# Optimization experiments

Measured on AMD Instinct MI355X. Metric: run time of the kernel, lower is better.

Reference implementation:

```python
import jax, jax.numpy as jnp
import numpy as np

VOCAB, EMBED_DIM, ENCODE_DIM = 50000, 128, 128
B, N = 512, 500            # trees per batch, nodes per tree
MAX_DEPTH = 40             # static bound on tree depth (uniform-attachment trees stay far below)


def setup_inputs() -> dict:
    rng = np.random.default_rng(0)
    T = B * N
    tokens = rng.integers(0, VOCAB, size=T).astype(np.int64)
    # random recursive trees: node i attaches to a uniformly random earlier node
    u = rng.random((B, N))
    pl = np.floor(u * np.arange(N)).astype(np.int64)  # local parent; node 0 is root
    depth = np.zeros((B, N), dtype=np.int64)
    rows = np.arange(B)
    for i in range(1, N):
        depth[:, i] = depth[rows, pl[:, i]] + 1
    assert depth.max() < MAX_DEPTH
    parent = pl + (np.arange(B)[:, None] * N)
    parent[:, 0] = T  # roots scatter into a dummy row
    node2batch = np.repeat(np.arange(B), N).astype(np.int64)

    key = jax.random.key(0)
    k1, k2, k3 = jax.random.split(key, 3)
    emb = jax.random.normal(k1, (VOCAB, EMBED_DIM), jnp.float32) * 0.02
    Wc = jax.random.normal(k2, (EMBED_DIM, ENCODE_DIM), jnp.float32) * 0.05
    bc = jax.random.normal(k3, (ENCODE_DIM,), jnp.float32) * 0.01
    return {
        "tokens": jnp.asarray(tokens),
        "parent": jnp.asarray(parent.reshape(-1)),
        "depth": jnp.asarray(depth.reshape(-1)),
        "node2batch": jnp.asarray(node2batch),
        "emb": emb, "Wc": Wc, "bc": bc, "bs": B,
    }


def reference(tokens, parent, depth, node2batch, emb, Wc, bc, bs):
    T = tokens.shape[0]
    # per-node W_c(embedding(token))  [T, D]
    x = emb[tokens] @ Wc + bc
    # bottom-up subtree sums: v(n) = sum_{m in subtree(n)} x[m]
    v = jnp.concatenate([x, jnp.zeros((1, x.shape[1]), x.dtype)], axis=0)  # +1 dummy row
    for d in range(MAX_DEPTH, 0, -1):
        contrib = jnp.where((depth == d)[:, None], v[:T], jnp.zeros((), x.dtype))
        v = v.at[parent].add(contrib)  # depth-d nodes push into depth d-1 parents
    node_vals = v[:T]
    # per-tree elementwise max over node values (node_list max-pool)
    out = jax.ops.segment_max(node_vals, node2batch, num_segments=bs)
    # rows absent from a node_list entry are zero, so the pool includes 0
    return jnp.maximum(out, jnp.zeros((), out.dtype))
```

## Files before the change

### kernel.cpp

```cpp
#include <hip/hip_runtime.h>
#include <hip/hip_bf16.h>

#define B_BATCH 512
#define NPB     500
#define DIM     128
#define VOCAB   50000
#define MAXD    40
#define NPREP   512
#define NGEMM   ((VOCAB + 63) / 64)

typedef short bf16x8 __attribute__((ext_vector_type(8)));
typedef float f32x4  __attribute__((ext_vector_type(4)));

__device__ __forceinline__ unsigned short f2bf(float x) {
    unsigned u = __float_as_uint(x);
    return (unsigned short)((u + 0x7fffu + ((u >> 16) & 1u)) >> 16);
}

__global__ __launch_bounds__(256, 3) void prep_gemm(const int* __restrict__ tokens,
                                                    const int* __restrict__ parent,
                                                    const int* __restrict__ depth,
                                                    const float* __restrict__ emb,
                                                    const float* __restrict__ Wc,
                                                    const float* __restrict__ bc,
                                                    int* __restrict__ tokD,
                                                    unsigned short* __restrict__ endD,
                                                    float* __restrict__ E) {
    __shared__ __align__(16) char smem[50176];
    const int tid = threadIdx.x;

    if (blockIdx.x >= NPREP) {
        unsigned short* sA = (unsigned short*)smem;
        unsigned short* sB = (unsigned short*)(smem + 17408);
        const int rowBase = (blockIdx.x - NPREP) * 64;

        for (int i = tid; i < DIM * DIM; i += 256) {
            int k = i >> 7, n = i & 127;
            int kc = k >> 5, q = (k >> 3) & 3, jj = k & 7;
            int nt = n >> 4, ln = q * 16 + (n & 15);
            sB[((kc * 8 + nt) * 64 + ln) * 8 + jj] = f2bf(Wc[i]);
        }
        for (int i = tid; i < 64 * 32; i += 256) {
            int r = i >> 5, k4 = (i & 31) * 4;
            float4 v = make_float4(0.f, 0.f, 0.f, 0.f);
            if (rowBase + r < VOCAB)
                v = *(const float4*)&emb[(long long)(rowBase + r) * DIM + k4];
            unsigned long long pk =  (unsigned long long)f2bf(v.x)
                                  | ((unsigned long long)f2bf(v.y) << 16)
                                  | ((unsigned long long)f2bf(v.z) << 32)
                                  | ((unsigned long long)f2bf(v.w) << 48);
            *(unsigned long long*)&sA[r * 136 + k4] = pk;
        }
        __syncthreads();

        const int lane = tid & 63, w = tid >> 6;
        const int q = lane >> 4, mc = lane & 15;

        f32x4 acc[8];
        #pragma unroll
        for (int nt = 0; nt < 8; ++nt) acc[nt] = (f32x4){0.f, 0.f, 0.f, 0.f};

        #pragma unroll
        for (int kc = 0; kc < 4; ++kc) {
            bf16x8 a = *(const bf16x8*)&sA[(w * 16 + mc) * 136 + kc * 32 + q * 8];
            #pragma unroll
            for (int nt = 0; nt < 8; ++nt) {
                bf16x8 bf = *(const bf16x8*)&sB[((kc * 8 + nt) * 64 + lane) * 8];
                acc[nt] = __builtin_amdgcn_mfma_f32_16x16x32_bf16(a, bf, acc[nt], 0, 0, 0);
            }
        }

        #pragma unroll
        for (int nt = 0; nt < 8; ++nt) {
            float bcv = bc[nt * 16 + mc];
            #pragma unroll
            for (int r = 0; r < 4; ++r) {
                int grow = rowBase + w * 16 + q * 4 + r;
                if (grow < VOCAB)
                    E[(long long)grow * DIM + nt * 16 + mc] = acc[nt][r] + bcv;
            }
        }
        return;
    }

    int*            sizeL  = (int*)smem;
    int*            pack   = (int*)(smem + 2000);
    int*            tokL   = (int*)(smem + 4000);
    int*            tmpTok = (int*)(smem + 6000);
    int*            hist   = (int*)(smem + 8000);
    int*            off    = (int*)(smem + 8164);
    int*            cur    = (int*)(smem + 8328);
    int*            sdmax  = (int*)(smem + 8492);
    unsigned short* parL   = (unsigned short*)(smem + 8496);
    unsigned short* depL   = (unsigned short*)(smem + 9496);
    unsigned short* sibp   = (unsigned short*)(smem + 10496);
    unsigned short* tinL   = (unsigned short*)(smem + 11496);
    unsigned short* bucket = (unsigned short*)(smem + 12496);
    unsigned short* tmpEnd = (unsigned short*)(smem + 13496);

    const int b = blockIdx.x;
    const long long base = (long long)b * NPB;

    if (tid <= MAXD) hist[tid] = 0;
    __syncthreads();
    for (int n = tid; n < NPB; n += 256) {
        int d = depth[base + n];
        depL[n]  = (unsigned short)d;
        parL[n]  = (unsigned short)(n == 0 ? 0 : (int)(parent[base + n] - base));
        tokL[n]  = tokens[base + n];
        sizeL[n] = 1;
        if (n > 0) atomicAdd(&hist[d], 1);
    }
    __syncthreads();

    if (tid < 64) {
        int h = (tid >= 1 && tid <= MAXD) ? hist[tid] : 0;
        int x = h;
        #pragma unroll
        for (int o = 1; o < 64; o <<= 1) { int y = __shfl_up(x, o, 64); if (tid >= o) x += y; }
        if (tid >= 1 && tid <= MAXD) { off[tid] = x - h; cur[tid] = x - h; }
        int dm = (h > 0) ? tid : 0;
        #pragma unroll
        for (int o = 32; o; o >>= 1) dm = max(dm, __shfl_down(dm, o));
        if (tid == 0) *sdmax = dm;
    }
    __syncthreads();

    for (int n = 1 + tid; n < NPB; n += 256)
        bucket[atomicAdd(&cur[depL[n]], 1)] = (unsigned short)n;
    __syncthreads();
    const int dmax = *sdmax;

    for (int d = dmax; d >= 1; --d) {
        int c = hist[d], o = off[d];
        for (int i = tid; i < c; i += 256) {
            int n = bucket[o + i];
            atomicAdd(&sizeL[parL[n]], sizeL[n]);
        }
        __syncthreads();
    }

    for (int n = tid; n < NPB; n += 256) pack[n] = (int)parL[n] | (sizeL[n] << 16);
    __syncthreads();

    {
        int n0 = tid, n1 = tid + 256;
        int p0 = parL[n0];
        int p1 = (n1 < NPB) ? parL[n1] : -1;
        int a0 = 0, a1 = 0;
        for (int m = 1; m < NPB; ++m) {
            int pk = pack[m];
            int pm = pk & 0xffff, sm = pk >> 16;
            if (m < n0 && pm == p0) a0 += sm;
            if (m < n1 && pm == p1) a1 += sm;
        }
        if (n0 >= 1) sibp[n0] = (unsigned short)a0;
        if (n1 >= 1 && n1 < NPB) sibp[n1] = (unsigned short)a1;
        if (tid == 0) tinL[0] = 0;
    }
    __syncthreads();

    for (int d = 1; d <= dmax; ++d) {
        int c = hist[d], o = off[d];
        for (int i = tid; i < c; i += 256) {
            int n = bucket[o + i];
            tinL[n] = (unsigned short)((int)tinL[parL[n]] + 1 + (int)sibp[n]);
        }
        __syncthreads();
    }

    for (int n = tid; n < NPB; n += 256) {
        int t = tinL[n];
        tmpTok[t] = tokL[n];
        tmpEnd[t] = (unsigned short)(t + sizeL[n] - 1);
    }
    __syncthreads();
    for (int t = tid; t < NPB; t += 256) {
        tokD[base + t] = tmpTok[t];
        endD[base + t] = tmpEnd[t];
    }
}

__global__ __launch_bounds__(512, 4) void scan_k(const int* __restrict__ tokD,
                                                 const unsigned short* __restrict__ endD,
                                                 const float* __restrict__ E,
                                                 float* __restrict__ out) {
    const int b = blockIdx.x & 511, s = blockIdx.x >> 9, tid = threadIdx.x;
    const long long base = (long long)b * NPB;
    __shared__ float S[NPB * 32];
    __shared__ int tokL[NPB];
    __shared__ unsigned short endL[NPB];
    __shared__ float partials[16 * 32];
    __shared__ float wmax[8 * 32];

    if (tid < NPB) {
        tokL[tid] = tokD[base + tid];
        endL[tid] = endD[base + tid];
    }
    __syncthreads();

    #pragma unroll
    for (int u = 0; u < 8; ++u) {
        int i = tid + u * 512;
        if (i < NPB * 8) {
            const float* g = &E[(long long)tokL[i >> 3] * DIM + s * 32 + (i & 7) * 4];
            __builtin_amdgcn_global_load_lds(
                (const __attribute__((address_space(1))) void*)g,
                (__attribute__((address_space(3))) void*)&S[i * 4], 16, 0, 0);
        }
    }
    __syncthreads();

    const int j = tid & 31, c = tid >> 5;
    float x[32];
    {
        float run = 0.f;
        #pragma unroll
        for (int k = 0; k < 32; ++k) {
            int t = c * 32 + k;
            float v = (t < NPB) ? S[t * 32 + j] : 0.f;
            run += v; x[k] = run;
        }
        partials[c * 32 + j] = run;
    }
    __syncthreads();
    float off = 0.f;
    for (int cc = 0; cc < c; ++cc) off += partials[cc * 32 + j];
    #pragma unroll
    for (int k = 0; k < 32; ++k) {
        int t = c * 32 + k;
        x[k] += off;
        if (t < NPB) S[t * 32 + j] = x[k];
    }
    __syncthreads();

    float m = -INFINITY;
    #pragma unroll
    for (int k = 0; k < 32; ++k) {
        int t = c * 32 + k;
        if (t < NPB) {
            float hi = S[(int)endL[t] * 32 + j];
            float lo = (k > 0) ? x[k - 1] : off;
            m = fmaxf(m, hi - lo);
        }
    }
    m = fmaxf(m, __shfl_down(m, 32));
    if ((tid & 63) < 32) wmax[(tid >> 6) * 32 + j] = m;
    __syncthreads();
    if (tid < 32) {
        float mm = wmax[tid];
        #pragma unroll
        for (int w = 1; w < 8; ++w) mm = fmaxf(mm, wmax[w * 32 + tid]);
        out[b * DIM + s * 32 + tid] = fmaxf(mm, 0.0f);
    }
}

extern "C" void kernel_launch(void* const* d_in, const int* in_sizes, int n_in,
                              void* d_out, int out_size, void* d_ws, size_t ws_size,
                              hipStream_t stream) {
    const int*   tokens = (const int*)d_in[0];
    const int*   parent = (const int*)d_in[1];
    const int*   depth  = (const int*)d_in[2];
    const float* emb    = (const float*)d_in[4];
    const float* Wc     = (const float*)d_in[5];
    const float* bc     = (const float*)d_in[6];
    float*       out    = (float*)d_out;

    float*          E    = (float*)d_ws;
    int*            tokD = (int*)(E + (long long)VOCAB * DIM);
    unsigned short* endD = (unsigned short*)(tokD + B_BATCH * NPB);

    prep_gemm<<<NPREP + NGEMM, 256, 0, stream>>>(tokens, parent, depth,
                                                 emb, Wc, bc, tokD, endD, E);
    scan_k<<<B_BATCH * 4, 512, 0, stream>>>(tokD, endD, E, out);
}
```

Measured before the change: 150.8 us.

## Split embedding GEMM into bf16 pre-swizzle pass and LDS-free MFMA kernel

The fused prep+GEMM kernel is split. A conversion pass writes the embedding table and Wc to workspace as bf16, already swizzled into MFMA fragment order. A separate GEMM kernel then loads fragments straight from global memory without staging in LDS or using barriers, and each GEMM block no longer re-converts Wc itself. The trade is an extra kernel launch plus a full bf16 round trip of the 50000x128 table through global memory.

```diff
diff --git a/kernel.cpp b/kernel.cpp
--- a/kernel.cpp
+++ b/kernel.cpp
@@ -7,7 +7,9 @@
 #define VOCAB   50000
 #define MAXD    40
 #define NPREP   512
+#define NCONV   768
 #define NGEMM   ((VOCAB + 63) / 64)
+#define EMB_OCT (VOCAB * 16)
 
 typedef short bf16x8 __attribute__((ext_vector_type(8)));
 typedef float f32x4  __attribute__((ext_vector_type(4)));
@@ -17,86 +19,53 @@
     return (unsigned short)((u + 0x7fffu + ((u >> 16) & 1u)) >> 16);
 }
 
-__global__ __launch_bounds__(256, 3) void prep_gemm(const int* __restrict__ tokens,
-                                                    const int* __restrict__ parent,
-                                                    const int* __restrict__ depth,
-                                                    const float* __restrict__ emb,
-                                                    const float* __restrict__ Wc,
-                                                    const float* __restrict__ bc,
-                                                    int* __restrict__ tokD,
-                                                    unsigned short* __restrict__ endD,
-                                                    float* __restrict__ E) {
-    __shared__ __align__(16) char smem[50176];
+__global__ __launch_bounds__(256) void conv_prep(const int* __restrict__ tokens,
+                                                 const int* __restrict__ parent,
+                                                 const int* __restrict__ depth,
+                                                 const float* __restrict__ emb,
+                                                 const float* __restrict__ Wc,
+                                                 int* __restrict__ tokD,
+                                                 unsigned short* __restrict__ endD,
+                                                 unsigned short* __restrict__ embB,
+                                                 unsigned short* __restrict__ WcB) {
     const int tid = threadIdx.x;
 
     if (blockIdx.x >= NPREP) {
-        unsigned short* sA = (unsigned short*)smem;
-        unsigned short* sB = (unsigned short*)(smem + 17408);
-        const int rowBase = (blockIdx.x - NPREP) * 64;
-
-        for (int i = tid; i < DIM * DIM; i += 256) {
-            int k = i >> 7, n = i & 127;
-            int kc = k >> 5, q = (k >> 3) & 3, jj = k & 7;
-            int nt = n >> 4, ln = q * 16 + (n & 15);
-            sB[((kc * 8 + nt) * 64 + ln) * 8 + jj] = f2bf(Wc[i]);
-        }
-        for (int i = tid; i < 64 * 32; i += 256) {
-            int r = i >> 5, k4 = (i & 31) * 4;
-            float4 v = make_float4(0.f, 0.f, 0.f, 0.f);
-            if (rowBase + r < VOCAB)
-                v = *(const float4*)&emb[(long long)(rowBase + r) * DIM + k4];
-            unsigned long long pk =  (unsigned long long)f2bf(v.x)
-                                  | ((unsigned long long)f2bf(v.y) << 16)
-                                  | ((unsigned long long)f2bf(v.z) << 32)
-                                  | ((unsigned long long)f2bf(v.w) << 48);
-            *(unsigned long long*)&sA[r * 136 + k4] = pk;
-        }
-        __syncthreads();
-
-        const int lane = tid & 63, w = tid >> 6;
-        const int q = lane >> 4, mc = lane & 15;
-
-        f32x4 acc[8];
-        #pragma unroll
-        for (int nt = 0; nt < 8; ++nt) acc[nt] = (f32x4){0.f, 0.f, 0.f, 0.f};
-
-        #pragma unroll
-        for (int kc = 0; kc < 4; ++kc) {
-            bf16x8 a = *(const bf16x8*)&sA[(w * 16 + mc) * 136 + kc * 32 + q * 8];
+        const int ct = (blockIdx.x - NPREP) * 256 + tid;
+        for (int i = ct; i < EMB_OCT; i += NCONV * 256) {
+            int r = ((i >> 8) << 4) | (i & 15);
+            int o = (i >> 4) & 15;
+            const float* src = &emb[(long long)r * DIM + o * 8];
+            float4 v0 = *(const float4*)src;
+            float4 v1 = *(const float4*)(src + 4);
+            unsigned short w[8] = {f2bf(v0.x), f2bf(v0.y), f2bf(v0.z), f2bf(v0.w),
+                                   f2bf(v1.x), f2bf(v1.y), f2bf(v1.z), f2bf(v1.w)};
+            *(bf16x8*)&embB[(long long)i * 8] = *(bf16x8*)w;
+        }
+        for (int i = ct; i < 2048; i += NCONV * 256) {
+            int kc = i >> 9, nt = (i >> 6) & 7, ln = i & 63;
+            int col   = (nt << 4) | (ln & 15);
+            int kbase = kc * 32 + (ln >> 4) * 8;
+            unsigned short w[8];
             #pragma unroll
-            for (int nt = 0; nt < 8; ++nt) {
-                bf16x8 bf = *(const bf16x8*)&sB[((kc * 8 + nt) * 64 + lane) * 8];
-                acc[nt] = __builtin_amdgcn_mfma_f32_16x16x32_bf16(a, bf, acc[nt], 0, 0, 0);
-            }
-        }
-
-        #pragma unroll
-        for (int nt = 0; nt < 8; ++nt) {
-            float bcv = bc[nt * 16 + mc];
-            #pragma unroll
-            for (int r = 0; r < 4; ++r) {
-                int grow = rowBase + w * 16 + q * 4 + r;
-                if (grow < VOCAB)
-                    E[(long long)grow * DIM + nt * 16 + mc] = acc[nt][r] + bcv;
-            }
+            for (int j = 0; j < 8; ++j) w[j] = f2bf(Wc[(kbase + j) * DIM + col]);
+            *(bf16x8*)&WcB[i * 8] = *(bf16x8*)w;
         }
         return;
     }
 
-    int*            sizeL  = (int*)smem;
-    int*            pack   = (int*)(smem + 2000);
-    int*            tokL   = (int*)(smem + 4000);
-    int*            tmpTok = (int*)(smem + 6000);
-    int*            hist   = (int*)(smem + 8000);
-    int*            off    = (int*)(smem + 8164);
-    int*            cur    = (int*)(smem + 8328);
-    int*            sdmax  = (int*)(smem + 8492);
-    unsigned short* parL   = (unsigned short*)(smem + 8496);
-    unsigned short* depL   = (unsigned short*)(smem + 9496);
-    unsigned short* sibp   = (unsigned short*)(smem + 10496);
-    unsigned short* tinL   = (unsigned short*)(smem + 11496);
-    unsigned short* bucket = (unsigned short*)(smem + 12496);
-    unsigned short* tmpEnd = (unsigned short*)(smem + 13496);
+    __shared__ unsigned short parL[NPB];
+    __shared__ unsigned short depL[NPB];
+    __shared__ int   tokL[NPB];
+    __shared__ int   sizeL[NPB];
+    __shared__ int   pack[NPB];
+    __shared__ unsigned short sibp[NPB];
+    __shared__ unsigned short tinL[NPB];
+    __shared__ unsigned short bucket[NPB];
+    __shared__ int hist[MAXD + 1], off[MAXD + 1], cur[MAXD + 1];
+    __shared__ int tmpTok[NPB];
+    __shared__ unsigned short tmpEnd[NPB];
+    __shared__ int sdmax;
 
     const int b = blockIdx.x;
     const long long base = (long long)b * NPB;
@@ -122,14 +91,14 @@
         int dm = (h > 0) ? tid : 0;
         #pragma unroll
         for (int o = 32; o; o >>= 1) dm = max(dm, __shfl_down(dm, o));
-        if (tid == 0) *sdmax = dm;
+        if (tid == 0) sdmax = dm;
     }
     __syncthreads();
 
     for (int n = 1 + tid; n < NPB; n += 256)
         bucket[atomicAdd(&cur[depL[n]], 1)] = (unsigned short)n;
     __syncthreads();
-    const int dmax = *sdmax;
+    const int dmax = sdmax;
 
     for (int d = dmax; d >= 1; --d) {
         int c = hist[d], o = off[d];
@@ -178,6 +147,45 @@
     for (int t = tid; t < NPB; t += 256) {
         tokD[base + t] = tmpTok[t];
         endD[base + t] = tmpEnd[t];
+    }
+}
+
+__global__ __launch_bounds__(256) void gemm_k(const unsigned short* __restrict__ embB,
+                                              const unsigned short* __restrict__ WcB,
+                                              const float* __restrict__ bc,
+                                              float* __restrict__ E) {
+    const int tid = threadIdx.x;
+    const int lane = tid & 63, w = tid >> 6;
+    const int q = lane >> 4, mc = lane & 15;
+    const long long tile = blockIdx.x;
+    const int rowBase = (int)tile * 64;
+
+    const bf16x8* Ao = (const bf16x8*)embB + (tile * 4 + w) * 256;
+    const bf16x8* Bo = (const bf16x8*)WcB;
+
+    f32x4 acc[8];
+    #pragma unroll
+    for (int nt = 0; nt < 8; ++nt) acc[nt] = (f32x4){0.f, 0.f, 0.f, 0.f};
+
+    #pragma unroll
+    for (int kc = 0; kc < 4; ++kc) {
+        bf16x8 a = Ao[(kc * 4 + q) * 16 + mc];
+        #pragma unroll
+        for (int nt = 0; nt < 8; ++nt) {
+            bf16x8 bf = Bo[(kc * 8 + nt) * 64 + lane];
+            acc[nt] = __builtin_amdgcn_mfma_f32_16x16x32_bf16(a, bf, acc[nt], 0, 0, 0);
+        }
+    }
+
+    #pragma unroll
+    for (int nt = 0; nt < 8; ++nt) {
+        float bcv = bc[nt * 16 + mc];
+        #pragma unroll
+        for (int r = 0; r < 4; ++r) {
+            int grow = rowBase + w * 16 + q * 4 + r;
+            if (grow < VOCAB)
+                E[(long long)grow * DIM + nt * 16 + mc] = acc[nt][r] + bcv;
+        }
     }
 }
 
@@ -267,10 +275,13 @@
     float*       out    = (float*)d_out;
 
     float*          E    = (float*)d_ws;
-    int*            tokD = (int*)(E + (long long)VOCAB * DIM);
+    unsigned short* embB = (unsigned short*)(E + (long long)VOCAB * DIM);
+    unsigned short* WcB  = embB + (long long)NGEMM * 64 * DIM;
+    int*            tokD = (int*)(WcB + DIM * DIM);
     unsigned short* endD = (unsigned short*)(tokD + B_BATCH * NPB);
 
-    prep_gemm<<<NPREP + NGEMM, 256, 0, stream>>>(tokens, parent, depth,
-                                                 emb, Wc, bc, tokD, endD, E);
+    conv_prep<<<NPREP + NCONV, 256, 0, stream>>>(tokens, parent, depth, emb, Wc,
+                                                 tokD, endD, embB, WcB);
+    gemm_k<<<NGEMM, 256, 0, stream>>>(embB, WcB, bc, E);
     scan_k<<<B_BATCH * 4, 512, 0, stream>>>(tokD, endD, E, out);
 }
```

New measurement: 156.6 us. 1.04x slower.
